# Kernel tuning notes

Measured on AMD Instinct MI355X. Metric: run time of the kernel, lower is better.

The kernel has to match this reference:

```python
import jax, jax.numpy as jnp
import numpy as np

C_CURV = 1.0  # hyperbolic curvature (init kwarg c)
EPS = 1e-7


def _to_ball(v, max_norm=0.8):
    # rescale rows to lie strictly inside the unit Poincare ball
    n = jnp.linalg.norm(v, axis=-1, keepdims=True)
    return v * (max_norm / (n + 1.0))


def setup_inputs() -> dict:
    key = jax.random.key(0)
    k1, k2 = jax.random.split(key)
    B, C, D = 32768, 2048, 512
    z_mix = _to_ball(jax.random.normal(k1, (B, D), dtype=jnp.float32))
    prototypes = _to_ball(jax.random.normal(k2, (C, D), dtype=jnp.float32))
    repel_margin = jnp.float32(2.0)
    return {"z_mix": z_mix, "prototypes": prototypes, "repel_margin": repel_margin}


def dist_matrix(x, y, c):
    # Poincare-ball pairwise distance (arccosh form):
    # d(x,y) = arccosh(1 + 2c||x-y||^2 / ((1-c||x||^2)(1-c||y||^2))) / sqrt(c)
    x2 = jnp.sum(x * x, axis=-1)            # (B,)
    y2 = jnp.sum(y * y, axis=-1)            # (C,)
    xy = jnp.einsum('bd,cd->bc', x, y)      # (B, C)
    sqdist = jnp.maximum(x2[:, None] + y2[None, :] - 2.0 * xy, 0.0)
    denom = (1.0 - c * x2)[:, None] * (1.0 - c * y2)[None, :]
    arg = 1.0 + 2.0 * c * sqdist / jnp.maximum(denom, EPS)
    return jnp.arccosh(jnp.maximum(arg, 1.0 + EPS)) / jnp.sqrt(c)


def reference(z_mix, prototypes, repel_margin):
    dist2proto = dist_matrix(z_mix, prototypes, C_CURV)   # (B, C)
    min_dist = jnp.min(dist2proto, axis=1)                # (B,)
    return jnp.mean(jax.nn.relu(repel_margin - min_dist))
```

## Files before the change

kernel.cpp:

```cpp
#include <hip/hip_runtime.h>
#include <stdint.h>

#define EPS_F 1e-7f

typedef float f32x4 __attribute__((ext_vector_type(4)));
typedef int   v8i   __attribute__((ext_vector_type(8)));

union A32 { uint4 u4[2]; v8i v; };

__device__ __forceinline__ unsigned cvt4(float a, float b, float c, float d) {
  int v = __builtin_amdgcn_cvt_pk_fp8_f32(a, b, 0, false);
  return (unsigned)__builtin_amdgcn_cvt_pk_fp8_f32(c, d, v, true);
}

#define MFMA128(A, B, C) __builtin_amdgcn_mfma_scale_f32_16x16x128_f8f6f4( \
    (A), (B), (C), 0, 0, 0, 0x7F7F7F7F, 0, 0x7F7F7F7F)


__global__ __launch_bounds__(256) void prep_kernel(
    const float* __restrict__ protos, uint8_t* __restrict__ wsB,
    float* __restrict__ y2a, float* __restrict__ rya,
    float* __restrict__ out) {
  const int lane = threadIdx.x & 63;
  const int w    = threadIdx.x >> 6;
  const int c    = blockIdx.x * 4 + w;
  const int g    = c >> 4, cl = c & 15;
  const float4* p = (const float4*)(protos + (size_t)c * 512 + lane * 8);
  float4 f0 = p[0], f1 = p[1];
  float s = f0.x*f0.x + f0.y*f0.y + f0.z*f0.z + f0.w*f0.w
          + f1.x*f1.x + f1.y*f1.y + f1.z*f1.z + f1.w*f1.w;
#pragma unroll
  for (int off = 32; off > 0; off >>= 1) s += __shfl_xor(s, off, 64);
  if (lane == 0) { y2a[c] = s; rya[c] = 1.f / (1.f - s); }
  unsigned ux = cvt4(f0.x, f0.y, f0.z, f0.w);
  unsigned uy = cvt4(f1.x, f1.y, f1.z, f1.w);
  const int kb = lane >> 4, kg = (lane >> 2) & 3, bo = lane & 3;
  size_t ri  = (size_t)(g * 4 + kb) * 64 + kg * 16 + cl;
  size_t off = ri * 16 + (size_t)(bo & 1) * 8 + (size_t)(bo >> 1) * (512u * 1024u);
  *(uint2*)(wsB + off) = make_uint2(ux, uy);
  if (blockIdx.x == 0 && threadIdx.x == 0) out[0] = 0.f;
}

__global__ __launch_bounds__(256, 1) void gemm_min_kernel(
    const float* __restrict__ z, const uint8_t* __restrict__ wsB,
    const float* __restrict__ y2a, const float* __restrict__ rya,
    const float* __restrict__ marg, float* __restrict__ out) {
  __shared__ uint4 AsLo[1024];
  __shared__ uint4 AsHi[1024];
  __shared__ float x2s[64];
  __shared__ float rxs[64];
  __shared__ float minbuf[64][4];

  const int tid  = threadIdx.x;
  const int lane = tid & 63;
  const int w    = tid >> 6;
  const int q    = lane >> 4;
  const int l15  = lane & 15;
  const size_t rowbase = (size_t)blockIdx.x * 64;

  const uint4* BLo = (const uint4*)wsB;
  const uint4* BHi = BLo + 32768;

  A32 Bp0[4], Bp1[4];
#pragma unroll
  for (int i = 0; i < 4; ++i) {
    size_t r0 = (size_t)(w * 128 + i) * 64 + lane;
    Bp0[i].u4[0] = BLo[r0];       Bp0[i].u4[1] = BHi[r0];
    Bp1[i].u4[0] = BLo[r0 + 256]; Bp1[i].u4[1] = BHi[r0 + 256];
  }

  {
    const float* rp0 = z + (rowbase + w * 16 + l15) * 512 + q * 128;
    float s = 0.f;
#pragma unroll
    for (int t = 0; t < 4; ++t) {
      const float4* rp = (const float4*)(rp0 + t * 32);
      float4 v0 = rp[0], v1 = rp[1], v2 = rp[2], v3 = rp[3];
      float4 v4 = rp[4], v5 = rp[5], v6 = rp[6], v7 = rp[7];
      s += v0.x*v0.x + v0.y*v0.y + v0.z*v0.z + v0.w*v0.w
         + v1.x*v1.x + v1.y*v1.y + v1.z*v1.z + v1.w*v1.w
         + v2.x*v2.x + v2.y*v2.y + v2.z*v2.z + v2.w*v2.w
         + v3.x*v3.x + v3.y*v3.y + v3.z*v3.z + v3.w*v3.w
         + v4.x*v4.x + v4.y*v4.y + v4.z*v4.z + v4.w*v4.w
         + v5.x*v5.x + v5.y*v5.y + v5.z*v5.z + v5.w*v5.w
         + v6.x*v6.x + v6.y*v6.y + v6.z*v6.z + v6.w*v6.w
         + v7.x*v7.x + v7.y*v7.y + v7.z*v7.z + v7.w*v7.w;
      uint4 lo, hi;
      lo.x = cvt4(v0.x, v0.y, v0.z, v0.w);
      lo.y = cvt4(v1.x, v1.y, v1.z, v1.w);
      lo.z = cvt4(v2.x, v2.y, v2.z, v2.w);
      lo.w = cvt4(v3.x, v3.y, v3.z, v3.w);
      hi.x = cvt4(v4.x, v4.y, v4.z, v4.w);
      hi.y = cvt4(v5.x, v5.y, v5.z, v5.w);
      hi.z = cvt4(v6.x, v6.y, v6.z, v6.w);
      hi.w = cvt4(v7.x, v7.y, v7.z, v7.w);
      int ri = (q * 4 + w) * 64 + t * 16 + l15;
      AsLo[ri] = lo; AsHi[ri] = hi;
    }
    s += __shfl_xor(s, 16, 64);
    s += __shfl_xor(s, 32, 64);
    if (lane < 16) { x2s[w * 16 + lane] = s; rxs[w * 16 + lane] = 1.f / (1.f - s); }
  }
  __syncthreads();

  float x2r[4][4];
#pragma unroll
  for (int rf = 0; rf < 4; ++rf) {
    float4 x4 = *(const float4*)&x2s[rf * 16 + q * 4];
    x2r[rf][0] = x4.x; x2r[rf][1] = x4.y; x2r[rf][2] = x4.z; x2r[rf][3] = x4.w;
  }

  float tmin[4][4];
#pragma unroll
  for (int rf = 0; rf < 4; ++rf)
#pragma unroll
    for (int r = 0; r < 4; ++r) tmin[rf][r] = 3.4e38f;

  const float* y2p = y2a + w * 512 + l15;
  const float* ryp = rya + w * 512 + l15;

#pragma clang loop unroll(disable)
  for (int s = 0; s < 16; ++s) {
    f32x4 acc[4][2];
#pragma unroll
    for (int rf = 0; rf < 4; ++rf) {
      f32x4 z4 = {0.f, 0.f, 0.f, 0.f};
      acc[rf][0] = z4; acc[rf][1] = z4;
    }
    float y2v0 = y2p[s * 32],      ryv0 = ryp[s * 32];
    float y2v1 = y2p[s * 32 + 16], ryv1 = ryp[s * 32 + 16];

#pragma unroll
    for (int kb = 0; kb < 4; ++kb) {
      v8i bv0 = Bp0[kb].v;
      v8i bv1 = Bp1[kb].v;
      {
        size_t r0 = ((size_t)(w * 32 + 2 * (s + 1)) * 4 + kb) * 64 + lane;
        Bp0[kb].u4[0] = BLo[r0];       Bp0[kb].u4[1] = BHi[r0];
        Bp1[kb].u4[0] = BLo[r0 + 256]; Bp1[kb].u4[1] = BHi[r0 + 256];
      }
#pragma unroll
      for (int rf = 0; rf < 4; ++rf) {
        A32 a;
        int ri = (kb * 4 + rf) * 64 + lane;
        a.u4[0] = AsLo[ri];
        a.u4[1] = AsHi[ri];
        acc[rf][0] = MFMA128(a.v, bv0, acc[rf][0]);
        acc[rf][1] = MFMA128(a.v, bv1, acc[rf][1]);
      }
    }

#pragma unroll
    for (int rf = 0; rf < 4; ++rf) {
#pragma unroll
      for (int r = 0; r < 4; ++r) {
        float xv = x2r[rf][r];
        float u0 = fmaxf(fmaf(-2.f, acc[rf][0][r], xv + y2v0), 0.f) * ryv0;
        float u1 = fmaxf(fmaf(-2.f, acc[rf][1][r], xv + y2v1), 0.f) * ryv1;
        tmin[rf][r] = fminf(tmin[rf][r], fminf(u0, u1));
      }
    }
  }

#pragma unroll
  for (int rf = 0; rf < 4; ++rf) {
#pragma unroll
    for (int r = 0; r < 4; ++r) {
      float v = tmin[rf][r];
      v = fminf(v, __shfl_xor(v, 1, 64));
      v = fminf(v, __shfl_xor(v, 2, 64));
      v = fminf(v, __shfl_xor(v, 4, 64));
      v = fminf(v, __shfl_xor(v, 8, 64));
      if (l15 == 0) minbuf[rf * 16 + q * 4 + r][w] = v;
    }
  }
  __syncthreads();

  if (w == 0) {
    float m = fminf(fminf(minbuf[lane][0], minbuf[lane][1]),
                    fminf(minbuf[lane][2], minbuf[lane][3]));
    float t = m * rxs[lane];
    float arg = fmaxf(fmaf(2.f, t, 1.f), 1.f + EPS_F);
    float contrib = fmaxf(marg[0] - acoshf(arg), 0.f);
#pragma unroll
    for (int off = 32; off > 0; off >>= 1) contrib += __shfl_xor(contrib, off, 64);
    if (lane == 0) atomicAdd(out, contrib * (1.0f / 32768.f));
  }
}

extern "C" void kernel_launch(void* const* d_in, const int* in_sizes, int n_in,
                              void* d_out, int out_size, void* d_ws, size_t ws_size,
                              hipStream_t stream) {
  const float* z      = (const float*)d_in[0];
  const float* protos = (const float*)d_in[1];
  const float* marg   = (const float*)d_in[2];
  float* out = (float*)d_out;
  uint8_t* wsB = (uint8_t*)d_ws;
  float* y2a = (float*)((char*)d_ws + (1 << 20) + 192 * 1024);
  float* rya = y2a + 2048;

  prep_kernel<<<512, 256, 0, stream>>>(protos, wsB, y2a, rya, out);
  gemm_min_kernel<<<512, 256, 0, stream>>>(z, wsB, y2a, rya, marg, out);
}
```

Before: 147.1 us.

## Split prototype columns across eight waves per block instead of four

Result: faster. 135.5 us (-7.9%).

```diff
diff --git a/kernel.cpp b/kernel.cpp
--- a/kernel.cpp
+++ b/kernel.cpp
@@ -41,7 +41,7 @@
   if (blockIdx.x == 0 && threadIdx.x == 0) out[0] = 0.f;
 }
 
-__global__ __launch_bounds__(256, 1) void gemm_min_kernel(
+__global__ __launch_bounds__(512, 1) void gemm_min_kernel(
     const float* __restrict__ z, const uint8_t* __restrict__ wsB,
     const float* __restrict__ y2a, const float* __restrict__ rya,
     const float* __restrict__ marg, float* __restrict__ out) {
@@ -49,7 +49,7 @@
   __shared__ uint4 AsHi[1024];
   __shared__ float x2s[64];
   __shared__ float rxs[64];
-  __shared__ float minbuf[64][4];
+  __shared__ float minbuf[64][8];
 
   const int tid  = threadIdx.x;
   const int lane = tid & 63;
@@ -61,15 +61,15 @@
   const uint4* BLo = (const uint4*)wsB;
   const uint4* BHi = BLo + 32768;
 
-  A32 Bp0[4], Bp1[4];
+  A32 Bp[4];
 #pragma unroll
   for (int i = 0; i < 4; ++i) {
-    size_t r0 = (size_t)(w * 128 + i) * 64 + lane;
-    Bp0[i].u4[0] = BLo[r0];       Bp0[i].u4[1] = BHi[r0];
-    Bp1[i].u4[0] = BLo[r0 + 256]; Bp1[i].u4[1] = BHi[r0 + 256];
-  }
-
-  {
+    size_t r0 = (size_t)(w * 64 + i) * 64 + lane;
+    Bp[i].u4[0] = BLo[r0];
+    Bp[i].u4[1] = BHi[r0];
+  }
+
+  if (w < 4) {
     const float* rp0 = z + (rowbase + w * 16 + l15) * 512 + q * 128;
     float s = 0.f;
 #pragma unroll
@@ -116,28 +116,26 @@
 #pragma unroll
     for (int r = 0; r < 4; ++r) tmin[rf][r] = 3.4e38f;
 
-  const float* y2p = y2a + w * 512 + l15;
-  const float* ryp = rya + w * 512 + l15;
+  const float* y2p = y2a + w * 256 + l15;
+  const float* ryp = rya + w * 256 + l15;
 
 #pragma clang loop unroll(disable)
   for (int s = 0; s < 16; ++s) {
-    f32x4 acc[4][2];
+    f32x4 acc[4];
 #pragma unroll
     for (int rf = 0; rf < 4; ++rf) {
       f32x4 z4 = {0.f, 0.f, 0.f, 0.f};
-      acc[rf][0] = z4; acc[rf][1] = z4;
-    }
-    float y2v0 = y2p[s * 32],      ryv0 = ryp[s * 32];
-    float y2v1 = y2p[s * 32 + 16], ryv1 = ryp[s * 32 + 16];
+      acc[rf] = z4;
+    }
+    float y2v = y2p[s * 16], ryv = ryp[s * 16];
 
 #pragma unroll
     for (int kb = 0; kb < 4; ++kb) {
-      v8i bv0 = Bp0[kb].v;
-      v8i bv1 = Bp1[kb].v;
+      v8i bv = Bp[kb].v;
       {
-        size_t r0 = ((size_t)(w * 32 + 2 * (s + 1)) * 4 + kb) * 64 + lane;
-        Bp0[kb].u4[0] = BLo[r0];       Bp0[kb].u4[1] = BHi[r0];
-        Bp1[kb].u4[0] = BLo[r0 + 256]; Bp1[kb].u4[1] = BHi[r0 + 256];
+        size_t r0 = ((size_t)(w * 16 + s + 1) * 4 + kb) * 64 + lane;
+        Bp[kb].u4[0] = BLo[r0];
+        Bp[kb].u4[1] = BHi[r0];
       }
 #pragma unroll
       for (int rf = 0; rf < 4; ++rf) {
@@ -145,8 +143,7 @@
         int ri = (kb * 4 + rf) * 64 + lane;
         a.u4[0] = AsLo[ri];
         a.u4[1] = AsHi[ri];
-        acc[rf][0] = MFMA128(a.v, bv0, acc[rf][0]);
-        acc[rf][1] = MFMA128(a.v, bv1, acc[rf][1]);
+        acc[rf] = MFMA128(a.v, bv, acc[rf]);
       }
     }
 
@@ -154,10 +151,8 @@
     for (int rf = 0; rf < 4; ++rf) {
 #pragma unroll
       for (int r = 0; r < 4; ++r) {
-        float xv = x2r[rf][r];
-        float u0 = fmaxf(fmaf(-2.f, acc[rf][0][r], xv + y2v0), 0.f) * ryv0;
-        float u1 = fmaxf(fmaf(-2.f, acc[rf][1][r], xv + y2v1), 0.f) * ryv1;
-        tmin[rf][r] = fminf(tmin[rf][r], fminf(u0, u1));
+        float u = fmaxf(fmaf(-2.f, acc[rf][r], x2r[rf][r] + y2v), 0.f) * ryv;
+        tmin[rf][r] = fminf(tmin[rf][r], u);
       }
     }
   }
@@ -177,8 +172,9 @@
   __syncthreads();
 
   if (w == 0) {
-    float m = fminf(fminf(minbuf[lane][0], minbuf[lane][1]),
-                    fminf(minbuf[lane][2], minbuf[lane][3]));
+    float m = minbuf[lane][0];
+#pragma unroll
+    for (int i = 1; i < 8; ++i) m = fminf(m, minbuf[lane][i]);
     float t = m * rxs[lane];
     float arg = fmaxf(fmaf(2.f, t, 1.f), 1.f + EPS_F);
     float contrib = fmaxf(marg[0] - acoshf(arg), 0.f);
@@ -200,5 +196,5 @@
   float* rya = y2a + 2048;
 
   prep_kernel<<<512, 256, 0, stream>>>(protos, wsB, y2a, rya, out);
-  gemm_min_kernel<<<512, 256, 0, stream>>>(z, wsB, y2a, rya, marg, out);
-}
+  gemm_min_kernel<<<512, 512, 0, stream>>>(z, wsB, y2a, rya, marg, out);
+}
```
